# Optimization experiments

Measured on AMD Instinct MI355X. Metric: run time of the kernel, lower is better.

## Reference

```python
import jax, jax.numpy as jnp
import numpy as np

N = 6            # Cl(6), Euclidean metric (+1,...,+1)
DIM = 2 ** N     # 64 blades
B = 256
IN_F = 16
HID = 64
NUM_GP = 4
EPS = 1e-6


def _build_algebra(n):
    dim = 2 ** n
    # grade-ordered basis: blades sorted by (grade, bitmask value)
    masks = sorted(range(dim), key=lambda m: (bin(m).count('1'), m))
    pos = {m: i for i, m in enumerate(masks)}
    cayley = np.zeros((dim, dim, dim), np.float32)  # C[i,j,k]: coeff of e_j in e_i*e_k
    for i, am in enumerate(masks):
        for k, bm in enumerate(masks):
            s, t = 0, am >> 1
            while t:  # canonical reordering sign (Euclidean: e_i^2=+1, no metric sign)
                s += bin(t & bm).count('1')
                t >>= 1
            cayley[i, pos[am ^ bm], k] = -1.0 if (s & 1) else 1.0
    qt = np.array([bin(m).count('1') % 4 for m in masks], np.int32)  # quaternion type = grade mod 4
    grade1 = np.array([i for i, m in enumerate(masks) if bin(m).count('1') == 1], np.int32)
    return cayley, qt, grade1

_C, _QT, _G1 = _build_algebra(N)
CAYLEY = jnp.asarray(_C)
QT = jnp.asarray(_QT)
G1 = jnp.asarray(_G1)
QT_ONEHOT = jax.nn.one_hot(_QT, 4, dtype=jnp.float32)  # (DIM,4)


def setup_inputs() -> dict:
    key = jax.random.key(0)
    ks = jax.random.split(key, 12)
    return {
        'points': jax.random.normal(ks[0], (B, IN_F, N), jnp.float32),
        'products': jax.random.normal(ks[1], (B,), jnp.float32),
        'lin_w': jax.random.normal(ks[2], (HID, IN_F, 4), jnp.float32) / np.sqrt(IN_F),
        'lin_b': jax.random.normal(ks[3], (HID,), jnp.float32) * 0.01,
        'gp_lin_w': jax.random.normal(ks[4], (NUM_GP, HID, HID, 4), jnp.float32) / np.sqrt(HID),
        'gp_a': jnp.zeros((NUM_GP, HID, 4), jnp.float32),
        'gp_w': jax.random.normal(ks[5], (NUM_GP, HID, 4, 4, 4), jnp.float32) / np.sqrt(DIM),
        'mlp_w1': jax.random.normal(ks[6], (HID, HID), jnp.float32) / np.sqrt(HID),
        'mlp_b1': jnp.zeros((HID,), jnp.float32),
        'mlp_w2': jax.random.normal(ks[7], (1, HID), jnp.float32) / np.sqrt(HID),
        'mlp_b2': jnp.zeros((1,), jnp.float32),
    }


def _qt_linear(x, w, b=None):
    # x: (B, m, DIM); w: (n_out, m, 4) shared across blades of same QT class
    wf = w[:, :, QT]  # (n_out, m, DIM)
    y = jnp.einsum('bmi,nmi->bni', x, wf)
    if b is not None:
        y = y.at[..., 0].add(b)  # bias on the scalar blade only
    return y


def _qt_normalize(x, a):
    # per-QT-class gated norm: x / (sigmoid(a)*(||x||_c - 1) + 1)
    sums = jnp.einsum('bfi,ic->bfc', x * x, QT_ONEHOT)        # (B,F,4)
    norms = jnp.sqrt(jnp.maximum(sums, 1e-12))
    norms = jax.nn.sigmoid(a) * (norms - 1.0) + 1.0
    return x / (norms[..., QT] + EPS)


def _qt_geometric_product(x, lw, a, w):
    # x: (B,F,DIM); lw: (F,F,4); a: (F,4); w: (F,4,4,4)
    xr = _qt_normalize(_qt_linear(x, lw), a)
    # expand QT-class weights to per-blade triples and modulate the Cayley table
    wfull = CAYLEY[None] * w[:, QT][:, :, QT][:, :, :, QT]     # (F,DIM,DIM,DIM)
    return jnp.einsum('bfi,fijk,bfk->bfj', x, wfull, xr)


def reference(points, products, lin_w, lin_b, gp_lin_w, gp_a, gp_w,
              mlp_w1, mlp_b1, mlp_w2, mlp_b2):
    # embed grade-1: put points into the n vector blades of the 2^n multivector
    x = jnp.zeros((B, IN_F, DIM), points.dtype).at[..., G1].set(points)
    x = _qt_linear(x, lin_w, lin_b)                            # (B,HID,DIM)
    for l in range(NUM_GP):
        x = _qt_geometric_product(x, gp_lin_w[l], gp_a[l], gp_w[l])
    y = jnp.linalg.norm(x, axis=-1)                            # (B,HID)
    h = jax.nn.silu(y @ mlp_w1.T + mlp_b1)
    pred = (h @ mlp_w2.T + mlp_b2)[..., 0]                     # (B,)
    loss = (pred - products) ** 2                              # mse, reduction='none'
    return loss.mean(), loss
```

## Files before the change

kernel.cpp:

```cpp
#include <hip/hip_runtime.h>

#define NB 256
#define IN_F 16
#define NGP 4

namespace alg {
constexpr int popc(int x){int c=0;while(x){c+=x&1;x>>=1;}return c;}
constexpr int qt(int m){return popc(m)&3;}
constexpr int sgn(int a,int b){int s=0;int t=a>>1;while(t){s+=popc(t&b);t>>=1;}return s&1;}
struct Tab {
  unsigned char w[64][64];
  unsigned char s[64][64];
};
constexpr Tab build(){
  Tab t{};
  for(int i=0;i<64;++i)for(int j=0;j<64;++j){
    int k=i^j;
    t.w[i][j]=(unsigned char)(qt(i)*16+qt(j)*4+qt(k));
    t.s[i][j]=(unsigned char)sgn(i,k);
  }
  return t;
}
constexpr Tab T = build();
}

__global__ void ga_prep(const float* __restrict__ gp_lin_w,
                        const float* __restrict__ gp_w,
                        const float* __restrict__ mlp_w1,
                        float* __restrict__ lw_t, float* __restrict__ gpw_t,
                        float* __restrict__ w1t,
                        float* __restrict__ out) {
  const int bx = blockIdx.x, t = threadIdx.x;
  if (bx == 0 && t == 0) out[0] = 0.f;
  if (bx < 256) {
    int o = bx*256 + t;
    int f = o & 63, m = (o>>6)&63, c = (o>>12)&3, l = (o>>14)&3;
    lw_t[o] = gp_lin_w[((l*64+f)*64+m)*4 + c];
  } else if (bx < 320) {
    int o = (bx-256)*256 + t;
    int f = o & 63, k = (o>>6)&63, l = (o>>12)&3;
    gpw_t[o] = gp_w[(l*64+f)*64 + k];
  } else {
    int o = (bx-320)*256 + t;
    int f = o & 63, f2 = o >> 6;
    w1t[o] = mlp_w1[f*64 + f2];
  }
}

template<int JO>
__device__ __forceinline__ void gp8(const float* __restrict__ x4,
                                    const float* __restrict__ y4,
                                    const float (&wv)[64], int f, float (&acc)[8]) {
  #pragma unroll
  for (int ic = 0; ic < 16; ++ic) {
    const float4 xv = *(const float4*)(x4 + (ic*64 + f)*4);
    const int r0 = ic ^ (2*JO);
    const float4 y0 = *(const float4*)(y4 + ( r0    *64 + f)*4);
    const float4 y1 = *(const float4*)(y4 + ((r0^1)*64 + f)*4);
    const float xa[4] = {xv.x, xv.y, xv.z, xv.w};
    const float ya[2][4] = {{y0.x,y0.y,y0.z,y0.w},{y1.x,y1.y,y1.z,y1.w}};
    #pragma unroll
    for (int h = 0; h < 2; ++h) {
      #pragma unroll
      for (int b = 0; b < 4; ++b) {
        const int j = 8*JO + 4*h + b;
        #pragma unroll
        for (int a = 0; a < 4; ++a) {
          const int i  = 4*ic + a;
          const int wi = alg::T.w[i][j];
          const float tp = wv[wi] * ya[h][a^b];
          acc[4*h+b] = alg::T.s[i][j] ? fmaf(-tp, xa[a], acc[4*h+b])
                                      : fmaf( tp, xa[a], acc[4*h+b]);
        }
      }
    }
  }
}

__global__ __launch_bounds__(512) void ga_main(
    const float* __restrict__ points, const float* __restrict__ products,
    const float* __restrict__ lin_w,  const float* __restrict__ lin_b,
    const float* __restrict__ gp_a,
    const float* __restrict__ mlp_b1,
    const float* __restrict__ mlp_w2, const float* __restrict__ mlp_b2,
    const float* __restrict__ lw_t,   const float* __restrict__ gpw_t,
    const float* __restrict__ w1t,
    float* __restrict__ d_out)
{
  __shared__ __align__(16) float x4[16*64*4];
  __shared__ __align__(16) float y4[16*64*4];
  __shared__ float red[4*8*64];
  __shared__ float invn[4*64];
  __shared__ float pts[96];
  __shared__ float ynrm[64];
  __shared__ float pad_lds[3072];

  const int t  = threadIdx.x;
  const int b  = blockIdx.x;
  const int f  = t & 63;
  const int jo = t >> 6;
  const int qb = __builtin_popcount((unsigned)jo) & 3;

  { volatile float* vp = pad_lds; vp[t] = 0.f; }

  for (int i = t; i < 16*64*4; i += 512) x4[i] = 0.f;
  if (t < 96) pts[t] = points[b*96 + t];
  __syncthreads();

  if (t < 64) {
    float a[6] = {0,0,0,0,0,0};
    for (int m = 0; m < IN_F; ++m) {
      float lw = lin_w[(t*IN_F+m)*4 + 1];
      #pragma unroll
      for (int g = 0; g < 6; ++g) a[g] = fmaf(pts[m*6+g], lw, a[g]);
    }
    x4[(0*64+t)*4+0] = lin_b[t];
    x4[(0*64+t)*4+1] = a[0];
    x4[(0*64+t)*4+2] = a[1];
    x4[(1*64+t)*4+0] = a[2];
    x4[(2*64+t)*4+0] = a[3];
    x4[(4*64+t)*4+0] = a[4];
    x4[(8*64+t)*4+0] = a[5];
  }
  __syncthreads();

  float acc[8];

  for (int l = 0; l < NGP; ++l) {
    float lacc[8] = {0,0,0,0,0,0,0,0};
    {
      const float* pA = lw_t + (l*4 + ((qb+0)&3))*4096 + f;
      const float* pB = lw_t + (l*4 + ((qb+1)&3))*4096 + f;
      const float* pC = lw_t + (l*4 + ((qb+2)&3))*4096 + f;
      const float* pD = lw_t + (l*4 + ((qb+3)&3))*4096 + f;
      #pragma unroll 8
      for (int m = 0; m < 64; ++m) {
        const float4 xq0 = *(const float4*)(x4 + ((2*jo  )*64 + m)*4);
        const float4 xq1 = *(const float4*)(x4 + ((2*jo+1)*64 + m)*4);
        const float wA = pA[m*64], wB = pB[m*64], wC = pC[m*64], wD = pD[m*64];
        lacc[0] = fmaf(wA, xq0.x, lacc[0]);
        lacc[1] = fmaf(wB, xq0.y, lacc[1]);
        lacc[2] = fmaf(wB, xq0.z, lacc[2]);
        lacc[3] = fmaf(wC, xq0.w, lacc[3]);
        lacc[4] = fmaf(wB, xq1.x, lacc[4]);
        lacc[5] = fmaf(wC, xq1.y, lacc[5]);
        lacc[6] = fmaf(wC, xq1.z, lacc[6]);
        lacc[7] = fmaf(wD, xq1.w, lacc[7]);
      }
    }
    *(float4*)(y4 + ((2*jo  )*64 + f)*4) = make_float4(lacc[0],lacc[1],lacc[2],lacc[3]);
    *(float4*)(y4 + ((2*jo+1)*64 + f)*4) = make_float4(lacc[4],lacc[5],lacc[6],lacc[7]);
    red[((qb+0)&3)*512 + jo*64 + f] = lacc[0]*lacc[0];
    red[((qb+1)&3)*512 + jo*64 + f] = lacc[1]*lacc[1] + lacc[2]*lacc[2] + lacc[4]*lacc[4];
    red[((qb+2)&3)*512 + jo*64 + f] = lacc[3]*lacc[3] + lacc[5]*lacc[5] + lacc[6]*lacc[6];
    red[((qb+3)&3)*512 + jo*64 + f] = lacc[7]*lacc[7];
    __syncthreads();

    if (t < 256) {
      const int cc = t >> 6, ff = t & 63;
      float s = 0.f;
      #pragma unroll
      for (int q = 0; q < 8; ++q) s += red[cc*512 + q*64 + ff];
      s = fmaxf(s, 1e-12f);
      float nrm = sqrtf(s);
      float av  = gp_a[(l*64+ff)*4 + cc];
      float sig = 1.f/(1.f + expf(-av));
      float nn  = sig*(nrm-1.f) + 1.f;
      invn[cc*64+ff] = 1.f/(nn + 1e-6f);
    }
    __syncthreads();

    float wv[64];
    {
      const float in0 = invn[0*64+f], in1 = invn[1*64+f],
                  in2 = invn[2*64+f], in3 = invn[3*64+f];
      const float* gw = gpw_t + l*4096 + f;
      #pragma unroll
      for (int wi = 0; wi < 64; ++wi) {
        const float sc = ((wi&3)==0)?in0:(((wi&3)==1)?in1:(((wi&3)==2)?in2:in3));
        wv[wi] = gw[wi*64] * sc;
      }
    }

    #pragma unroll
    for (int ii = 0; ii < 8; ++ii) acc[ii] = 0.f;
    switch (jo) {
      case 0: gp8<0>(x4, y4, wv, f, acc); break;
      case 1: gp8<1>(x4, y4, wv, f, acc); break;
      case 2: gp8<2>(x4, y4, wv, f, acc); break;
      case 3: gp8<3>(x4, y4, wv, f, acc); break;
      case 4: gp8<4>(x4, y4, wv, f, acc); break;
      case 5: gp8<5>(x4, y4, wv, f, acc); break;
      case 6: gp8<6>(x4, y4, wv, f, acc); break;
      default: gp8<7>(x4, y4, wv, f, acc); break;
    }
    __syncthreads();
    if (l < NGP-1) {
      *(float4*)(x4 + ((2*jo  )*64 + f)*4) = make_float4(acc[0],acc[1],acc[2],acc[3]);
      *(float4*)(x4 + ((2*jo+1)*64 + f)*4) = make_float4(acc[4],acc[5],acc[6],acc[7]);
    }
    __syncthreads();
  }

  float ss = 0.f;
  #pragma unroll
  for (int ii = 0; ii < 8; ++ii) ss = fmaf(acc[ii], acc[ii], ss);
  red[jo*64+f] = ss;
  __syncthreads();
  if (t < 64) {
    float s = 0.f;
    #pragma unroll
    for (int q = 0; q < 8; ++q) s += red[q*64+t];
    ynrm[t] = sqrtf(s);
  }
  __syncthreads();
  {
    float hp = 0.f;
    #pragma unroll
    for (int d = 0; d < 8; ++d) {
      const int f2 = 8*jo + d;
      hp = fmaf(w1t[f2*64+f], ynrm[f2], hp);
    }
    red[jo*64+f] = hp;
  }
  __syncthreads();
  if (t < 64) {
    float hpre = mlp_b1[t];
    #pragma unroll
    for (int q = 0; q < 8; ++q) hpre += red[q*64+t];
    float h = hpre / (1.f + expf(-hpre));
    float p = h * mlp_w2[t];
    #pragma unroll
    for (int off = 32; off > 0; off >>= 1) p += __shfl_down(p, off, 64);
    if (t == 0) {
      float pred = p + mlp_b2[0];
      float d = pred - products[b];
      float loss = d*d;
      d_out[1+b] = loss;
      atomicAdd(d_out, loss * (1.f/256.f));
    }
  }
}

extern "C" void kernel_launch(void* const* d_in, const int* in_sizes, int n_in,
                              void* d_out, int out_size, void* d_ws, size_t ws_size,
                              hipStream_t stream) {
  const float* points   = (const float*)d_in[0];
  const float* products = (const float*)d_in[1];
  const float* lin_w    = (const float*)d_in[2];
  const float* lin_b    = (const float*)d_in[3];
  const float* gp_lin_w = (const float*)d_in[4];
  const float* gp_a     = (const float*)d_in[5];
  const float* gp_w     = (const float*)d_in[6];
  const float* mlp_w1   = (const float*)d_in[7];
  const float* mlp_b1   = (const float*)d_in[8];
  const float* mlp_w2   = (const float*)d_in[9];
  const float* mlp_b2   = (const float*)d_in[10];
  float* out = (float*)d_out;

  float* lw_t  = (float*)d_ws;
  float* gpw_t = lw_t + 65536;
  float* w1t   = gpw_t + 16384;

  ga_prep<<<336, 256, 0, stream>>>(gp_lin_w, gp_w, mlp_w1, lw_t, gpw_t, w1t, out);
  ga_main<<<NB, 512, 0, stream>>>(points, products, lin_w, lin_b, gp_a,
                                  mlp_b1, mlp_w2, mlp_b2,
                                  lw_t, gpw_t, w1t, out);
}
```

Baseline: 126.3 us.

## Split per-thread work to 4 output blades with 1024-thread blocks

Doubles the threads per block from 512 to 1024 so each thread computes 4 output blades instead of 8 in both the QT-linear and geometric-product stages. The norm-reduction buffer is reorganized into a per-blade-quad layout, and the padding LDS grows. The prep kernel is rewritten so reads are coalesced and writes are scattered. The aim is more parallelism and fewer registers per thread (smaller accumulators), at the cost of more wavefronts per block, more redundant weight loads, and a larger LDS footprint that limits occupancy.

```diff
diff --git a/kernel.cpp b/kernel.cpp
--- a/kernel.cpp
+++ b/kernel.cpp
@@ -33,51 +33,47 @@
   const int bx = blockIdx.x, t = threadIdx.x;
   if (bx == 0 && t == 0) out[0] = 0.f;
   if (bx < 256) {
-    int o = bx*256 + t;
-    int f = o & 63, m = (o>>6)&63, c = (o>>12)&3, l = (o>>14)&3;
-    lw_t[o] = gp_lin_w[((l*64+f)*64+m)*4 + c];
+    const int l = bx >> 6, f = bx & 63;
+    const int m = t >> 2, c = t & 3;
+    lw_t[((l*4+c)*64 + m)*64 + f] = gp_lin_w[bx*256 + t];
   } else if (bx < 320) {
-    int o = (bx-256)*256 + t;
-    int f = o & 63, k = (o>>6)&63, l = (o>>12)&3;
-    gpw_t[o] = gp_w[(l*64+f)*64 + k];
+    const int b2 = bx - 256;
+    const int l = b2 >> 4, f0 = (b2 & 15) * 4;
+    const int f = f0 + (t >> 6), k = t & 63;
+    gpw_t[(l*64 + k)*64 + f] = gp_w[(l*64 + f0)*64 + t];
   } else {
-    int o = (bx-320)*256 + t;
-    int f = o & 63, f2 = o >> 6;
-    w1t[o] = mlp_w1[f*64 + f2];
-  }
-}
-
-template<int JO>
-__device__ __forceinline__ void gp8(const float* __restrict__ x4,
+    const int o = (bx - 320)*256 + t;
+    const int f = o >> 6, f2 = o & 63;
+    w1t[f2*64 + f] = mlp_w1[o];
+  }
+}
+
+template<int JQ>
+__device__ __forceinline__ void gp4(const float* __restrict__ x4,
                                     const float* __restrict__ y4,
-                                    const float (&wv)[64], int f, float (&acc)[8]) {
+                                    const float (&wv)[64], int f, float (&acc)[4]) {
   #pragma unroll
   for (int ic = 0; ic < 16; ++ic) {
     const float4 xv = *(const float4*)(x4 + (ic*64 + f)*4);
-    const int r0 = ic ^ (2*JO);
-    const float4 y0 = *(const float4*)(y4 + ( r0    *64 + f)*4);
-    const float4 y1 = *(const float4*)(y4 + ((r0^1)*64 + f)*4);
+    const float4 yv = *(const float4*)(y4 + ((ic^JQ)*64 + f)*4);
     const float xa[4] = {xv.x, xv.y, xv.z, xv.w};
-    const float ya[2][4] = {{y0.x,y0.y,y0.z,y0.w},{y1.x,y1.y,y1.z,y1.w}};
-    #pragma unroll
-    for (int h = 0; h < 2; ++h) {
-      #pragma unroll
-      for (int b = 0; b < 4; ++b) {
-        const int j = 8*JO + 4*h + b;
-        #pragma unroll
-        for (int a = 0; a < 4; ++a) {
-          const int i  = 4*ic + a;
-          const int wi = alg::T.w[i][j];
-          const float tp = wv[wi] * ya[h][a^b];
-          acc[4*h+b] = alg::T.s[i][j] ? fmaf(-tp, xa[a], acc[4*h+b])
-                                      : fmaf( tp, xa[a], acc[4*h+b]);
-        }
+    const float ya[4] = {yv.x, yv.y, yv.z, yv.w};
+    #pragma unroll
+    for (int b = 0; b < 4; ++b) {
+      #pragma unroll
+      for (int a = 0; a < 4; ++a) {
+        const int i  = 4*ic + a;
+        const int j  = 4*JQ + b;
+        const int wi = alg::T.w[i][j];
+        const float tp = wv[wi] * ya[a^b];
+        acc[b] = alg::T.s[i][j] ? fmaf(-tp, xa[a], acc[b])
+                                : fmaf( tp, xa[a], acc[b]);
       }
     }
   }
 }
 
-__global__ __launch_bounds__(512) void ga_main(
+__global__ __launch_bounds__(1024) void ga_main(
     const float* __restrict__ points, const float* __restrict__ products,
     const float* __restrict__ lin_w,  const float* __restrict__ lin_b,
     const float* __restrict__ gp_a,
@@ -89,21 +85,22 @@
 {
   __shared__ __align__(16) float x4[16*64*4];
   __shared__ __align__(16) float y4[16*64*4];
-  __shared__ float red[4*8*64];
+  __shared__ __align__(16) float red4[16*64*4];
   __shared__ float invn[4*64];
   __shared__ float pts[96];
   __shared__ float ynrm[64];
-  __shared__ float pad_lds[3072];
+  __shared__ float pad_lds[8448];
 
   const int t  = threadIdx.x;
   const int b  = blockIdx.x;
   const int f  = t & 63;
-  const int jo = t >> 6;
-  const int qb = __builtin_popcount((unsigned)jo) & 3;
+  const int jq = t >> 6;
+  const int qj = __builtin_popcount((unsigned)jq) & 3;
+  const int cA = qj, cB = (qj+1)&3, cC = (qj+2)&3, cD = (qj+3)&3;
 
   { volatile float* vp = pad_lds; vp[t] = 0.f; }
 
-  for (int i = t; i < 16*64*4; i += 512) x4[i] = 0.f;
+  for (int i = t; i < 16*64*4; i += 1024) x4[i] = 0.f;
   if (t < 96) pts[t] = points[b*96 + t];
   __syncthreads();
 
@@ -124,43 +121,36 @@
   }
   __syncthreads();
 
-  float acc[8];
+  float acc[4];
 
   for (int l = 0; l < NGP; ++l) {
-    float lacc[8] = {0,0,0,0,0,0,0,0};
+    float lacc[4] = {0,0,0,0};
     {
-      const float* pA = lw_t + (l*4 + ((qb+0)&3))*4096 + f;
-      const float* pB = lw_t + (l*4 + ((qb+1)&3))*4096 + f;
-      const float* pC = lw_t + (l*4 + ((qb+2)&3))*4096 + f;
-      const float* pD = lw_t + (l*4 + ((qb+3)&3))*4096 + f;
+      const float* pA = lw_t + (l*4 + cA)*4096 + f;
+      const float* pB = lw_t + (l*4 + cB)*4096 + f;
+      const float* pC = lw_t + (l*4 + cC)*4096 + f;
       #pragma unroll 8
       for (int m = 0; m < 64; ++m) {
-        const float4 xq0 = *(const float4*)(x4 + ((2*jo  )*64 + m)*4);
-        const float4 xq1 = *(const float4*)(x4 + ((2*jo+1)*64 + m)*4);
-        const float wA = pA[m*64], wB = pB[m*64], wC = pC[m*64], wD = pD[m*64];
-        lacc[0] = fmaf(wA, xq0.x, lacc[0]);
-        lacc[1] = fmaf(wB, xq0.y, lacc[1]);
-        lacc[2] = fmaf(wB, xq0.z, lacc[2]);
-        lacc[3] = fmaf(wC, xq0.w, lacc[3]);
-        lacc[4] = fmaf(wB, xq1.x, lacc[4]);
-        lacc[5] = fmaf(wC, xq1.y, lacc[5]);
-        lacc[6] = fmaf(wC, xq1.z, lacc[6]);
-        lacc[7] = fmaf(wD, xq1.w, lacc[7]);
+        const float4 xq = *(const float4*)(x4 + (jq*64 + m)*4);
+        const float wA = pA[m*64], wB = pB[m*64], wC = pC[m*64];
+        lacc[0] = fmaf(wA, xq.x, lacc[0]);
+        lacc[1] = fmaf(wB, xq.y, lacc[1]);
+        lacc[2] = fmaf(wB, xq.z, lacc[2]);
+        lacc[3] = fmaf(wC, xq.w, lacc[3]);
       }
     }
-    *(float4*)(y4 + ((2*jo  )*64 + f)*4) = make_float4(lacc[0],lacc[1],lacc[2],lacc[3]);
-    *(float4*)(y4 + ((2*jo+1)*64 + f)*4) = make_float4(lacc[4],lacc[5],lacc[6],lacc[7]);
-    red[((qb+0)&3)*512 + jo*64 + f] = lacc[0]*lacc[0];
-    red[((qb+1)&3)*512 + jo*64 + f] = lacc[1]*lacc[1] + lacc[2]*lacc[2] + lacc[4]*lacc[4];
-    red[((qb+2)&3)*512 + jo*64 + f] = lacc[3]*lacc[3] + lacc[5]*lacc[5] + lacc[6]*lacc[6];
-    red[((qb+3)&3)*512 + jo*64 + f] = lacc[7]*lacc[7];
+    *(float4*)(y4 + (jq*64 + f)*4) = make_float4(lacc[0],lacc[1],lacc[2],lacc[3]);
+    red4[(jq*64+f)*4 + cA] = lacc[0]*lacc[0];
+    red4[(jq*64+f)*4 + cB] = lacc[1]*lacc[1] + lacc[2]*lacc[2];
+    red4[(jq*64+f)*4 + cC] = lacc[3]*lacc[3];
+    red4[(jq*64+f)*4 + cD] = 0.f;
     __syncthreads();
 
     if (t < 256) {
       const int cc = t >> 6, ff = t & 63;
       float s = 0.f;
       #pragma unroll
-      for (int q = 0; q < 8; ++q) s += red[cc*512 + q*64 + ff];
+      for (int q = 0; q < 16; ++q) s += red4[(q*64+ff)*4 + cc];
       s = fmaxf(s, 1e-12f);
       float nrm = sqrtf(s);
       float av  = gp_a[(l*64+ff)*4 + cc];
@@ -183,51 +173,59 @@
     }
 
     #pragma unroll
-    for (int ii = 0; ii < 8; ++ii) acc[ii] = 0.f;
-    switch (jo) {
-      case 0: gp8<0>(x4, y4, wv, f, acc); break;
-      case 1: gp8<1>(x4, y4, wv, f, acc); break;
-      case 2: gp8<2>(x4, y4, wv, f, acc); break;
-      case 3: gp8<3>(x4, y4, wv, f, acc); break;
-      case 4: gp8<4>(x4, y4, wv, f, acc); break;
-      case 5: gp8<5>(x4, y4, wv, f, acc); break;
-      case 6: gp8<6>(x4, y4, wv, f, acc); break;
-      default: gp8<7>(x4, y4, wv, f, acc); break;
+    for (int ii = 0; ii < 4; ++ii) acc[ii] = 0.f;
+    switch (jq) {
+      case  0: gp4< 0>(x4, y4, wv, f, acc); break;
+      case  1: gp4< 1>(x4, y4, wv, f, acc); break;
+      case  2: gp4< 2>(x4, y4, wv, f, acc); break;
+      case  3: gp4< 3>(x4, y4, wv, f, acc); break;
+      case  4: gp4< 4>(x4, y4, wv, f, acc); break;
+      case  5: gp4< 5>(x4, y4, wv, f, acc); break;
+      case  6: gp4< 6>(x4, y4, wv, f, acc); break;
+      case  7: gp4< 7>(x4, y4, wv, f, acc); break;
+      case  8: gp4< 8>(x4, y4, wv, f, acc); break;
+      case  9: gp4< 9>(x4, y4, wv, f, acc); break;
+      case 10: gp4<10>(x4, y4, wv, f, acc); break;
+      case 11: gp4<11>(x4, y4, wv, f, acc); break;
+      case 12: gp4<12>(x4, y4, wv, f, acc); break;
+      case 13: gp4<13>(x4, y4, wv, f, acc); break;
+      case 14: gp4<14>(x4, y4, wv, f, acc); break;
+      default: gp4<15>(x4, y4, wv, f, acc); break;
     }
     __syncthreads();
     if (l < NGP-1) {
-      *(float4*)(x4 + ((2*jo  )*64 + f)*4) = make_float4(acc[0],acc[1],acc[2],acc[3]);
-      *(float4*)(x4 + ((2*jo+1)*64 + f)*4) = make_float4(acc[4],acc[5],acc[6],acc[7]);
+      *(float4*)(x4 + (jq*64 + f)*4) = make_float4(acc[0],acc[1],acc[2],acc[3]);
     }
     __syncthreads();
   }
 
   float ss = 0.f;
   #pragma unroll
-  for (int ii = 0; ii < 8; ++ii) ss = fmaf(acc[ii], acc[ii], ss);
-  red[jo*64+f] = ss;
+  for (int ii = 0; ii < 4; ++ii) ss = fmaf(acc[ii], acc[ii], ss);
+  red4[jq*64+f] = ss;
   __syncthreads();
   if (t < 64) {
     float s = 0.f;
     #pragma unroll
-    for (int q = 0; q < 8; ++q) s += red[q*64+t];
+    for (int q = 0; q < 16; ++q) s += red4[q*64+t];
     ynrm[t] = sqrtf(s);
   }
   __syncthreads();
   {
     float hp = 0.f;
     #pragma unroll
-    for (int d = 0; d < 8; ++d) {
-      const int f2 = 8*jo + d;
+    for (int d = 0; d < 4; ++d) {
+      const int f2 = 4*jq + d;
       hp = fmaf(w1t[f2*64+f], ynrm[f2], hp);
     }
-    red[jo*64+f] = hp;
+    __syncthreads();
+    red4[jq*64+f] = hp;
   }
   __syncthreads();
   if (t < 64) {
     float hpre = mlp_b1[t];
     #pragma unroll
-    for (int q = 0; q < 8; ++q) hpre += red[q*64+t];
+    for (int q = 0; q < 16; ++q) hpre += red4[q*64+t];
     float h = hpre / (1.f + expf(-hpre));
     float p = h * mlp_w2[t];
     #pragma unroll
@@ -263,7 +261,7 @@
   float* w1t   = gpw_t + 16384;
 
   ga_prep<<<336, 256, 0, stream>>>(gp_lin_w, gp_w, mlp_w1, lw_t, gpw_t, w1t, out);
-  ga_main<<<NB, 512, 0, stream>>>(points, products, lin_w, lin_b, gp_a,
-                                  mlp_b1, mlp_w2, mlp_b2,
-                                  lw_t, gpw_t, w1t, out);
-}
+  ga_main<<<NB, 1024, 0, stream>>>(points, products, lin_w, lin_b, gp_a,
+                                   mlp_b1, mlp_w2, mlp_b2,
+                                   lw_t, gpw_t, w1t, out);
+}
```

Result: slower. 227.6 us (+80.2%).
